# Kernel optimization log

Measured on AMD Instinct MI355X. Metric: run time of the kernel, lower is better.

## Reference

```python
import jax, jax.numpy as jnp
import numpy as np
from jax import lax

B, T, D, NH = 8, 2048, 128, 4
HD = D // NH
EPS = 1e-5


def _ln(x, g, b):
    m = x.mean(-1, keepdims=True)
    v = ((x - m) ** 2).mean(-1, keepdims=True)
    return (x - m) / jnp.sqrt(v + EPS) * g + b


def _gelu(x):  # exact (erf) GELU, matching torch nn.GELU default
    return jax.nn.gelu(x, approximate=False)


def _forward(lob_feat, trade_feat, has_trade,
             ei_w, ei_b, ei_g, ei_beta, decay,
             in_proj_w, in_proj_b, out_proj_w, out_proj_b,
             cn_g, cn_b,
             lob_w, lob_b, lob_g, lob_beta,
             tr_w, tr_b, tr_g, tr_beta,
             of_w, of_b, of_g, of_beta):
    # event impact: Linear -> LayerNorm -> Tanh, gated by has_trade
    impact = jnp.tanh(_ln(trade_feat @ ei_w.T + ei_b, ei_g, ei_beta))
    impact = impact * has_trade[..., None]              # [B,T,D]

    # diagonal linear recurrence: state_t = sigmoid(decay) * state_{t-1} + impact_t
    d = jax.nn.sigmoid(decay)                           # [D]

    def step(s, x):
        s = d * s + x
        return s, s

    _, states = lax.scan(step, jnp.zeros_like(impact[:, 0]),
                         jnp.swapaxes(impact, 0, 1))    # [T,B,D]
    state_seq = jnp.swapaxes(states, 0, 1)              # [B,T,D]

    # fusion MLPs (dropout is identity in eval)
    lob_enh = _gelu(_ln(jnp.concatenate([lob_feat, state_seq], -1) @ lob_w.T + lob_b,
                        lob_g, lob_beta))
    trade_enh = _gelu(_ln(jnp.concatenate([trade_feat, state_seq], -1) @ tr_w.T + tr_b,
                          tr_g, tr_beta))

    # torch nn.MultiheadAttention (batch_first): q=lob_enh, k=v=trade_enh
    wq, wk, wv = in_proj_w[:D], in_proj_w[D:2 * D], in_proj_w[2 * D:]
    bq, bk, bv = in_proj_b[:D], in_proj_b[D:2 * D], in_proj_b[2 * D:]
    q = (lob_enh @ wq.T + bq).reshape(B, T, NH, HD)
    k = (trade_enh @ wk.T + bk).reshape(B, T, NH, HD)
    v = (trade_enh @ wv.T + bv).reshape(B, T, NH, HD)
    scores = jnp.einsum('bqhd,bkhd->bhqk', q, k) / jnp.sqrt(jnp.float32(HD))
    attn = jax.nn.softmax(scores, axis=-1)
    ctx = jnp.einsum('bhqk,bkhd->bqhd', attn, v).reshape(B, T, D)
    fused_attn = ctx @ out_proj_w.T + out_proj_b

    fused = _ln(lob_enh + fused_attn, cn_g, cn_b)
    output = _gelu(_ln(jnp.concatenate([fused, trade_enh], -1) @ of_w.T + of_b,
                       of_g, of_beta))
    return output


def setup_inputs() -> dict:
    key = jax.random.key(0)
    ks = jax.random.split(key, 20)
    s1 = 1.0 / np.sqrt(D)
    s2 = 1.0 / np.sqrt(2 * D)
    return {
        'lob_feat': jax.random.normal(ks[0], (B, T, D), jnp.float32),
        'trade_feat': jax.random.normal(ks[1], (B, T, D), jnp.float32),
        'has_trade': (jax.random.uniform(ks[2], (B, T)) < 0.5).astype(jnp.float32),
        'ei_w': jax.random.normal(ks[3], (D, D), jnp.float32) * s1,
        'ei_b': jnp.zeros((D,), jnp.float32),
        'ei_g': jnp.ones((D,), jnp.float32),
        'ei_beta': jnp.zeros((D,), jnp.float32),
        'decay': jnp.ones((D,), jnp.float32) * 0.9,
        'in_proj_w': jax.random.normal(ks[4], (3 * D, D), jnp.float32) * s1,
        'in_proj_b': jnp.zeros((3 * D,), jnp.float32),
        'out_proj_w': jax.random.normal(ks[5], (D, D), jnp.float32) * s1,
        'out_proj_b': jnp.zeros((D,), jnp.float32),
        'cn_g': jnp.ones((D,), jnp.float32),
        'cn_b': jnp.zeros((D,), jnp.float32),
        'lob_w': jax.random.normal(ks[6], (D, 2 * D), jnp.float32) * s2,
        'lob_b': jnp.zeros((D,), jnp.float32),
        'lob_g': jnp.ones((D,), jnp.float32),
        'lob_beta': jnp.zeros((D,), jnp.float32),
        'tr_w': jax.random.normal(ks[7], (D, 2 * D), jnp.float32) * s2,
        'tr_b': jnp.zeros((D,), jnp.float32),
        'tr_g': jnp.ones((D,), jnp.float32),
        'tr_beta': jnp.zeros((D,), jnp.float32),
        'of_w': jax.random.normal(ks[8], (D, 2 * D), jnp.float32) * s2,
        'of_b': jnp.zeros((D,), jnp.float32),
        'of_g': jnp.ones((D,), jnp.float32),
        'of_beta': jnp.zeros((D,), jnp.float32),
    }


def reference(lob_feat, trade_feat, has_trade,
              ei_w, ei_b, ei_g, ei_beta, decay,
              in_proj_w, in_proj_b, out_proj_w, out_proj_b,
              cn_g, cn_b,
              lob_w, lob_b, lob_g, lob_beta,
              tr_w, tr_b, tr_g, tr_beta,
              of_w, of_b, of_g, of_beta):
    return _forward(lob_feat, trade_feat, has_trade,
                    ei_w, ei_b, ei_g, ei_beta, decay,
                    in_proj_w, in_proj_b, out_proj_w, out_proj_b,
                    cn_g, cn_b,
                    lob_w, lob_b, lob_g, lob_beta,
                    tr_w, tr_b, tr_g, tr_beta,
                    of_w, of_b, of_g, of_beta)
```

## Files before the change

kernel.cpp:

```cpp
#include <hip/hip_runtime.h>
#include <math.h>


#define T_  2048

typedef short bf16x8 __attribute__((ext_vector_type(8)));
typedef float f32x4  __attribute__((ext_vector_type(4)));
typedef unsigned short ushort_t;

__device__ __forceinline__ float sigm(float x) { return 1.0f / (1.0f + __expf(-x)); }

__device__ __forceinline__ unsigned short f2bf(float x) {
    union { float f; unsigned u; } v; v.f = x;
    unsigned r = v.u + 0x7FFFu + ((v.u >> 16) & 1u);
    return (unsigned short)(r >> 16);
}
__device__ __forceinline__ float bf2f(ushort_t u) {
    union { unsigned u; float f; } v; v.u = ((unsigned)u) << 16; return v.f;
}

__device__ __forceinline__ float gelu_f(float x) {
    const float e = exp2f(fmaf(0.044715f * x, x * x, x) * -2.3022083f);
    return x * __builtin_amdgcn_rcpf(1.0f + e);
}
__device__ __forceinline__ float tanh_f(float y) {
    const float e = exp2f(y * 2.8853900818f);
    return 1.0f - 2.0f * __builtin_amdgcn_rcpf(e + 1.0f);
}
#define MX3(a, b, c) fmaxf(fmaxf((a), (b)), (c))

__global__ __launch_bounds__(256) void prep_kernel(
    const float* __restrict__ lob, const float* __restrict__ trade,
    const float* __restrict__ eiw, const float* __restrict__ ipw,
    const float* __restrict__ opw, const float* __restrict__ lobw,
    const float* __restrict__ trw, const float* __restrict__ ofw,
    ushort_t* __restrict__ pool)
{
    const size_t i8 = ((size_t)blockIdx.x * 256 + threadIdx.x) * 8;
    const float* src; size_t off;
    if      (i8 < 2097152) { src = lob;   off = 0; }
    else if (i8 < 4194304) { src = trade; off = 2097152; }
    else if (i8 < 4210688) { src = eiw;   off = 4194304; }
    else if (i8 < 4259840) { src = ipw;   off = 4210688; }
    else if (i8 < 4276224) { src = opw;   off = 4259840; }
    else if (i8 < 4308992) { src = lobw;  off = 4276224; }
    else if (i8 < 4341760) { src = trw;   off = 4308992; }
    else                   { src = ofw;   off = 4341760; }
    const float4 a = *(const float4*)(src + (i8 - off));
    const float4 b = *(const float4*)(src + (i8 - off) + 4);
    bf16x8 o;
    o[0] = (short)f2bf(a.x); o[1] = (short)f2bf(a.y);
    o[2] = (short)f2bf(a.z); o[3] = (short)f2bf(a.w);
    o[4] = (short)f2bf(b.x); o[5] = (short)f2bf(b.y);
    o[6] = (short)f2bf(b.z); o[7] = (short)f2bf(b.w);
    *(bf16x8*)(pool + i8) = o;
}

__global__ __launch_bounds__(256) void gemm_ei(
    const ushort_t* __restrict__ Xb0, const ushort_t* __restrict__ Wb,
    const float* __restrict__ bias, const float* __restrict__ gamma,
    const float* __restrict__ beta, const float* __restrict__ extra,
    ushort_t* __restrict__ outb)
{
    __shared__ float red[32][2][2];
    const int tid = threadIdx.x, wid = tid >> 6, lane = tid & 63;
    const int c2 = lane & 15, g = lane >> 4;
    const int rowblk = wid >> 1, chf = wid & 1, cb0 = chf * 4;
    const int R0 = blockIdx.x * 32 + rowblk * 16;

    f32x4 acc[4] = {};
#pragma unroll
    for (int ch = 0; ch < 4; ch++) {
        const bf16x8 a = *(const bf16x8*)(Xb0 + (size_t)(R0 + c2) * 128 + ch * 32 + g * 8);
#pragma unroll
        for (int j = 0; j < 4; j++) {
            const bf16x8 b = *(const bf16x8*)(Wb + (size_t)((cb0 + j) * 16 + c2) * 128 + ch * 32 + g * 8);
            acc[j] = __builtin_amdgcn_mfma_f32_16x16x32_bf16(a, b, acc[j], 0, 0, 0);
        }
    }
    float gm[4], bt[4];
#pragma unroll
    for (int j = 0; j < 4; j++) {
        const int col = (cb0 + j) * 16 + c2;
        const float bb = bias[col];
        gm[j] = gamma[col]; bt[j] = beta[col];
#pragma unroll
        for (int r = 0; r < 4; r++) acc[j][r] += bb;
    }
#pragma unroll
    for (int r = 0; r < 4; r++) {
        float s = 0.f, ss = 0.f;
#pragma unroll
        for (int j = 0; j < 4; j++) { const float v = acc[j][r]; s += v; ss = fmaf(v, v, ss); }
#pragma unroll
        for (int o = 8; o; o >>= 1) { s += __shfl_xor(s, o); ss += __shfl_xor(ss, o); }
        if (c2 == 0) {
            red[rowblk * 16 + 4 * g + r][chf][0] = s;
            red[rowblk * 16 + 4 * g + r][chf][1] = ss;
        }
    }
    __syncthreads();
#pragma unroll
    for (int r = 0; r < 4; r++) {
        const int lr = rowblk * 16 + 4 * g + r;
        const float S  = red[lr][0][0] + red[lr][1][0];
        const float SS = red[lr][0][1] + red[lr][1][1];
        const float mean = S * (1.0f / 128.0f);
        float var = SS * (1.0f / 128.0f) - mean * mean;
        var = fmaxf(var, 0.0f);
        const float rstd = rsqrtf(var + 1e-5f);
        const int R = blockIdx.x * 32 + lr;
        const float ext = extra[R];
#pragma unroll
        for (int j = 0; j < 4; j++) {
            const float y = (acc[j][r] - mean) * rstd * gm[j] + bt[j];
            outb[(size_t)R * 128 + (cb0 + j) * 16 + c2] = f2bf(tanh_f(y) * ext);
        }
    }
}

__global__ __launch_bounds__(256) void enh_qkv(
    const ushort_t* __restrict__ lobb, const ushort_t* __restrict__ trab,
    const ushort_t* __restrict__ stab,
    const ushort_t* __restrict__ lobw, const ushort_t* __restrict__ trw,
    const ushort_t* __restrict__ ipw, const float* __restrict__ ipb,
    const float* __restrict__ lob_b, const float* __restrict__ lob_g,
    const float* __restrict__ lob_beta,
    const float* __restrict__ tr_b, const float* __restrict__ tr_g,
    const float* __restrict__ tr_beta,
    ushort_t* __restrict__ lobe_b, ushort_t* __restrict__ tre_bf,
    ushort_t* __restrict__ qo, ushort_t* __restrict__ ko, ushort_t* __restrict__ vo)
{
    __shared__ ushort_t lob_t[32][136];
    __shared__ ushort_t tre_t[32][136];
    __shared__ ushort_t vls[128][36];
    __shared__ float red[32][2][4];
    const int tid = threadIdx.x, wid = tid >> 6, lane = tid & 63;
    const int c2 = lane & 15, g = lane >> 4;
    const int rowblk = wid >> 1, chf = wid & 1, cb0 = chf * 4;
    const int RB = blockIdx.x * 32;
    const int R0 = RB + rowblk * 16;

    f32x4 aL[4] = {}, aT[4] = {};
#pragma unroll
    for (int ch = 0; ch < 8; ch++) {
        const int kk = (ch & 3) * 32;
        bf16x8 xl, xt;
        if (ch < 4) {
            xl = *(const bf16x8*)(lobb + (size_t)(R0 + c2) * 128 + kk + g * 8);
            xt = *(const bf16x8*)(trab + (size_t)(R0 + c2) * 128 + kk + g * 8);
        } else {
            xl = *(const bf16x8*)(stab + (size_t)(R0 + c2) * 128 + kk + g * 8);
            xt = xl;
        }
#pragma unroll
        for (int j = 0; j < 4; j++) {
            const size_t wo = (size_t)((cb0 + j) * 16 + c2) * 256 + ch * 32 + g * 8;
            aL[j] = __builtin_amdgcn_mfma_f32_16x16x32_bf16(xl, *(const bf16x8*)(lobw + wo), aL[j], 0, 0, 0);
            aT[j] = __builtin_amdgcn_mfma_f32_16x16x32_bf16(xt, *(const bf16x8*)(trw + wo), aT[j], 0, 0, 0);
        }
    }
#pragma unroll
    for (int j = 0; j < 4; j++) {
        const int col = (cb0 + j) * 16 + c2;
        const float bL = lob_b[col], bT = tr_b[col];
#pragma unroll
        for (int r = 0; r < 4; r++) { aL[j][r] += bL; aT[j][r] += bT; }
    }
#pragma unroll
    for (int r = 0; r < 4; r++) {
        float sL = 0.f, ssL = 0.f, sT = 0.f, ssT = 0.f;
#pragma unroll
        for (int j = 0; j < 4; j++) {
            const float vL = aL[j][r], vT = aT[j][r];
            sL += vL; ssL = fmaf(vL, vL, ssL);
            sT += vT; ssT = fmaf(vT, vT, ssT);
        }
#pragma unroll
        for (int o = 8; o; o >>= 1) {
            sL += __shfl_xor(sL, o); ssL += __shfl_xor(ssL, o);
            sT += __shfl_xor(sT, o); ssT += __shfl_xor(ssT, o);
        }
        if (c2 == 0) {
            float* rd = red[rowblk * 16 + 4 * g + r][chf];
            rd[0] = sL; rd[1] = ssL; rd[2] = sT; rd[3] = ssT;
        }
    }
    __syncthreads();
#pragma unroll
    for (int r = 0; r < 4; r++) {
        const int lr = rowblk * 16 + 4 * g + r;
        const int R = RB + lr;
        const float SL  = red[lr][0][0] + red[lr][1][0];
        const float SSL = red[lr][0][1] + red[lr][1][1];
        const float ST  = red[lr][0][2] + red[lr][1][2];
        const float SST = red[lr][0][3] + red[lr][1][3];
        const float mL = SL * (1.0f / 128.0f), mT = ST * (1.0f / 128.0f);
        const float rL = rsqrtf(fmaxf(SSL * (1.0f / 128.0f) - mL * mL, 0.0f) + 1e-5f);
        const float rT = rsqrtf(fmaxf(SST * (1.0f / 128.0f) - mT * mT, 0.0f) + 1e-5f);
#pragma unroll
        for (int j = 0; j < 4; j++) {
            const int col = (cb0 + j) * 16 + c2;
            const float yL = gelu_f((aL[j][r] - mL) * rL * lob_g[col] + lob_beta[col]);
// ... 3 lines not shown
            lob_t[lr][col] = lb;
            const ushort_t tb = f2bf(yT);
            tre_bf[(size_t)R * 128 + col] = tb;
            tre_t[lr][col] = tb;
        }
    }
    __syncthreads();

    const float qscale = 0.17677669529663687f * 1.4426950408889634f;
#pragma unroll
    for (int which = 0; which < 3; which++) {
        const ushort_t (*src)[136] = (which == 0) ? lob_t : tre_t;
        const ushort_t* Wp = ipw + (size_t)which * 16384;
        f32x4 pa[4] = {};
#pragma unroll
        for (int ch = 0; ch < 4; ch++) {
            const bf16x8 a = *(const bf16x8*)&src[rowblk * 16 + c2][ch * 32 + g * 8];
#pragma unroll
            for (int j = 0; j < 4; j++) {
                const bf16x8 b = *(const bf16x8*)(Wp + (size_t)((cb0 + j) * 16 + c2) * 128 + ch * 32 + g * 8);
                pa[j] = __builtin_amdgcn_mfma_f32_16x16x32_bf16(a, b, pa[j], 0, 0, 0);
            }
        }
        if (which < 2) {
            ushort_t* dst = (which == 0) ? qo : ko;
            const float sc = (which == 0) ? qscale : 1.0f;
#pragma unroll
            for (int j = 0; j < 4; j++) {
                const int col = (cb0 + j) * 16 + c2;
                const float bb = ipb[which * 128 + col];
                const int h = col >> 5, hd = col & 31;
#pragma unroll
                for (int r = 0; r < 4; r++) {
                    const int R = R0 + 4 * g + r;
                    const int b = R >> 11, t = R & 2047;
                    dst[(((size_t)b * 4 + h) * 2048 + t) * 32 + hd] = f2bf((pa[j][r] + bb) * sc);
                }
            }
        } else {
#pragma unroll
            for (int j = 0; j < 4; j++) {
                const int col = (cb0 + j) * 16 + c2;
                const float bb = ipb[256 + col];
#pragma unroll
                for (int r = 0; r < 4; r++)
                    vls[col][rowblk * 16 + 4 * g + r] = f2bf(pa[j][r] + bb);
            }
        }
    }
    __syncthreads();
    {
        const int col = tid >> 1, hf = tid & 1;
        const int h = col >> 5, hd = col & 31;
        const int b = RB >> 11;
        unsigned w[8];
#pragma unroll
        for (int e = 0; e < 8; e++) {
            const int p0 = hf * 16 + 2 * e;
            const int g2 = p0 >> 3, j2 = p0 & 7;
            const int lk = 4 * g2 + j2 + (j2 >= 4 ? 12 : 0);
            w[e] = (unsigned)vls[col][lk] | ((unsigned)vls[col][lk + 1] << 16);
        }
        ushort_t* dst = vo + (((size_t)b * 4 + h) * 32 + hd) * 2048 + (RB & 2047) + hf * 16;
        *(uint4*)dst       = *(const uint4*)&w[0];
        *(uint4*)(dst + 8) = *(const uint4*)&w[4];
    }
}

__global__ __launch_bounds__(256) void attn_kernel(
    const ushort_t* __restrict__ q, const ushort_t* __restrict__ k,
    const ushort_t* __restrict__ vtg,
    ushort_t* __restrict__ part, float* __restrict__ rs_part,
    float* __restrict__ m_part)
{
    __shared__ ushort_t ks[2][64][40];
    __shared__ ushort_t vt[2][32][72];
    const int tid = threadIdx.x, wid = tid >> 6, lane = tid & 63;
    const int c = lane & 15, g = lane >> 4;
    const int half = blockIdx.x & 1, qt = blockIdx.x >> 1;
    const int bh = blockIdx.y, b = bh >> 2, h = bh & 3;
    const ushort_t* kb_ = k   + (size_t)bh * 65536 + (size_t)half * 1024 * 32;
    const ushort_t* vb_ = vtg + (size_t)bh * 65536 + (size_t)half * 1024;
    const int q0 = qt * 128 + wid * 32;

    const ushort_t* qbase = q + ((size_t)bh * 2048 + q0) * 32;
    const bf16x8 qf0 = *(const bf16x8*)(qbase + (size_t)c * 32 + g * 8);
    const bf16x8 qf1 = *(const bf16x8*)(qbase + (size_t)(16 + c) * 32 + g * 8);

    bf16x8 ones;
#pragma unroll
    for (int i = 0; i < 8; i++) ones[i] = (short)0x3F80;

    float m0 = 0.0f, m1 = 0.0f;
    f32x4 acc[2][2] = {};
    f32x4 racc[2] = {};

    const int srow = tid >> 2, ssg = tid & 3;
    const int vd = tid >> 3, vkg = tid & 7;

    {
        const bf16x8 kk8 = *(const bf16x8*)(kb_ + (size_t)srow * 32 + ssg * 8);
        const bf16x8 vv8 = *(const bf16x8*)(vb_ + (size_t)vd * 2048 + vkg * 8);
        *(bf16x8*)&ks[0][srow][ssg * 8] = kk8;
        *(bf16x8*)&vt[0][vd][vkg * 8] = vv8;
    }
    __syncthreads();

    for (int kt = 0; kt < 16; kt++) {
        const int cur = kt & 1;
        bf16x8 kk8, vv8;
        if (kt + 1 < 16) {
            kk8 = *(const bf16x8*)(kb_ + ((size_t)(kt + 1) * 64 + srow) * 32 + ssg * 8);
            vv8 = *(const bf16x8*)(vb_ + (size_t)vd * 2048 + (kt + 1) * 64 + vkg * 8);
        }

        f32x4 s0[4], s1[4];
        __builtin_amdgcn_s_setprio(1);
#pragma unroll
        for (int kb2 = 0; kb2 < 4; kb2++) {
            const bf16x8 kf = *(const bf16x8*)&ks[cur][kb2 * 16 + c][g * 8];
            f32x4 z = {};
            s0[kb2] = __builtin_amdgcn_mfma_f32_16x16x32_bf16(kf, qf0, z, 0, 0, 0);
            s1[kb2] = __builtin_amdgcn_mfma_f32_16x16x32_bf16(kf, qf1, z, 0, 0, 0);
        }
        __builtin_amdgcn_s_setprio(0);

        float lm = MX3(s0[0][0], s0[0][1], s0[0][2]);
        lm = MX3(lm, s0[0][3], s0[1][0]);
        lm = MX3(lm, s0[1][1], s0[1][2]);
        lm = MX3(lm, s0[1][3], s0[2][0]);
        lm = MX3(lm, s0[2][1], s0[2][2]);
        lm = MX3(lm, s0[2][3], s0[3][0]);
        lm = MX3(lm, s0[3][1], s0[3][2]);
        lm = MX3(lm, s0[3][3], s1[0][0]);
        lm = MX3(lm, s1[0][1], s1[0][2]);
        lm = MX3(lm, s1[0][3], s1[1][0]);
        lm = MX3(lm, s1[1][1], s1[1][2]);
        lm = MX3(lm, s1[1][3], s1[2][0]);
        lm = MX3(lm, s1[2][1], s1[2][2]);
        lm = MX3(lm, s1[2][3], s1[3][0]);
        lm = MX3(lm, s1[3][1], s1[3][2]);
        lm = fmaxf(lm, s1[3][3]);
        if (__any(lm > 80.0f || m0 != 0.0f || m1 != 0.0f)) {
            float l0 = -1e30f, l1 = -1e30f;
#pragma unroll
            for (int kb2 = 0; kb2 < 4; kb2++) {
#pragma unroll
                for (int r = 0; r < 4; r++) { l0 = fmaxf(l0, s0[kb2][r]); l1 = fmaxf(l1, s1[kb2][r]); }
            }
            l0 = fmaxf(l0, __shfl_xor(l0, 16)); l0 = fmaxf(l0, __shfl_xor(l0, 32));
            l1 = fmaxf(l1, __shfl_xor(l1, 16)); l1 = fmaxf(l1, __shfl_xor(l1, 32));
            const float n0 = fmaxf(m0, l0), n1 = fmaxf(m1, l1);
            const float a0 = exp2f(m0 - n0), a1 = exp2f(m1 - n1);
#pragma unroll
            for (int nb = 0; nb < 2; nb++)
#pragma unroll
                for (int r = 0; r < 4; r++) { acc[0][nb][r] *= a0; acc[1][nb][r] *= a1; }
#pragma unroll
            for (int r = 0; r < 4; r++) { racc[0][r] *= a0; racc[1][r] *= a1; }
            m0 = n0; m1 = n1;
#pragma unroll
            for (int kb2 = 0; kb2 < 4; kb2++)
#pragma unroll
                for (int r = 0; r < 4; r++) {
                    s0[kb2][r] = exp2f(s0[kb2][r] - m0);
                    s1[kb2][r] = exp2f(s1[kb2][r] - m1);
                }
        } else {
#pragma unroll
            for (int kb2 = 0; kb2 < 4; kb2++)
#pragma unroll
                for (int r = 0; r < 4; r++) {
                    s0[kb2][r] = exp2f(s0[kb2][r]);
                    s1[kb2][r] = exp2f(s1[kb2][r]);
                }
        }

        union { unsigned u[4]; bf16x8 v; } p0a, p0b, p1a, p1b;
        asm("v_cvt_pk_bf16_f32 %0, %1, %2" : "=v"(p0a.u[0]) : "v"(s0[0][0]), "v"(s0[0][1]));
        asm("v_cvt_pk_bf16_f32 %0, %1, %2" : "=v"(p0a.u[1]) : "v"(s0[0][2]), "v"(s0[0][3]));
        asm("v_cvt_pk_bf16_f32 %0, %1, %2" : "=v"(p0a.u[2]) : "v"(s0[1][0]), "v"(s0[1][1]));
        asm("v_cvt_pk_bf16_f32 %0, %1, %2" : "=v"(p0a.u[3]) : "v"(s0[1][2]), "v"(s0[1][3]));
        asm("v_cvt_pk_bf16_f32 %0, %1, %2" : "=v"(p0b.u[0]) : "v"(s0[2][0]), "v"(s0[2][1]));
        asm("v_cvt_pk_bf16_f32 %0, %1, %2" : "=v"(p0b.u[1]) : "v"(s0[2][2]), "v"(s0[2][3]));
        asm("v_cvt_pk_bf16_f32 %0, %1, %2" : "=v"(p0b.u[2]) : "v"(s0[3][0]), "v"(s0[3][1]));
        asm("v_cvt_pk_bf16_f32 %0, %1, %2" : "=v"(p0b.u[3]) : "v"(s0[3][2]), "v"(s0[3][3]));
        asm("v_cvt_pk_bf16_f32 %0, %1, %2" : "=v"(p1a.u[0]) : "v"(s1[0][0]), "v"(s1[0][1]));
        asm("v_cvt_pk_bf16_f32 %0, %1, %2" : "=v"(p1a.u[1]) : "v"(s1[0][2]), "v"(s1[0][3]));
        asm("v_cvt_pk_bf16_f32 %0, %1, %2" : "=v"(p1a.u[2]) : "v"(s1[1][0]), "v"(s1[1][1]));
        asm("v_cvt_pk_bf16_f32 %0, %1, %2" : "=v"(p1a.u[3]) : "v"(s1[1][2]), "v"(s1[1][3]));
        asm("v_cvt_pk_bf16_f32 %0, %1, %2" : "=v"(p1b.u[0]) : "v"(s1[2][0]), "v"(s1[2][1]));
        asm("v_cvt_pk_bf16_f32 %0, %1, %2" : "=v"(p1b.u[1]) : "v"(s1[2][2]), "v"(s1[2][3]));
        asm("v_cvt_pk_bf16_f32 %0, %1, %2" : "=v"(p1b.u[2]) : "v"(s1[3][0]), "v"(s1[3][1]));
        asm("v_cvt_pk_bf16_f32 %0, %1, %2" : "=v"(p1b.u[3]) : "v"(s1[3][2]), "v"(s1[3][3]));

        __builtin_amdgcn_s_setprio(1);
#pragma unroll
        for (int nb = 0; nb < 2; nb++) {
            const bf16x8 v0 = *(const bf16x8*)&vt[cur][nb * 16 + c][g * 8];
            const bf16x8 v1 = *(const bf16x8*)&vt[cur][nb * 16 + c][32 + g * 8];
            acc[0][nb] = __builtin_amdgcn_mfma_f32_16x16x32_bf16(v0, p0a.v, acc[0][nb], 0, 0, 0);
            acc[0][nb] = __builtin_amdgcn_mfma_f32_16x16x32_bf16(v1, p0b.v, acc[0][nb], 0, 0, 0);
            acc[1][nb] = __builtin_amdgcn_mfma_f32_16x16x32_bf16(v0, p1a.v, acc[1][nb], 0, 0, 0);
            acc[1][nb] = __builtin_amdgcn_mfma_f32_16x16x32_bf16(v1, p1b.v, acc[1][nb], 0, 0, 0);
        }
        racc[0] = __builtin_amdgcn_mfma_f32_16x16x32_bf16(ones, p0a.v, racc[0], 0, 0, 0);
        racc[0] = __builtin_amdgcn_mfma_f32_16x16x32_bf16(ones, p0b.v, racc[0], 0, 0, 0);
        racc[1] = __builtin_amdgcn_mfma_f32_16x16x32_bf16(ones, p1a.v, racc[1], 0, 0, 0);
        racc[1] = __builtin_amdgcn_mfma_f32_16x16x32_bf16(ones, p1b.v, racc[1], 0, 0, 0);
        __builtin_amdgcn_s_setprio(0);

        if (kt + 1 < 16) {
            *(bf16x8*)&ks[cur ^ 1][srow][ssg * 8] = kk8;
            *(bf16x8*)&vt[cur ^ 1][vd][vkg * 8] = vv8;
        }
        __syncthreads();
    }

    ushort_t* pb = part + (size_t)half * 2097152;
#pragma unroll
    for (int qf = 0; qf < 2; qf++) {
        const int qrow = q0 + qf * 16 + c;
        ushort_t* dst = pb + ((size_t)(b * 2048 + qrow)) * 128 + h * 32;
#pragma unroll
        for (int nb = 0; nb < 2; nb++) {
            unsigned w0, w1;
            asm("v_cvt_pk_bf16_f32 %0, %1, %2" : "=v"(w0) : "v"(acc[qf][nb][0]), "v"(acc[qf][nb][1]));
            asm("v_cvt_pk_bf16_f32 %0, %1, %2" : "=v"(w1) : "v"(acc[qf][nb][2]), "v"(acc[qf][nb][3]));
            uint2 wv; wv.x = w0; wv.y = w1;
            *(uint2*)(dst + nb * 16 + 4 * g) = wv;
        }
    }
    if (g == 0) {
        float* rsp = rs_part + (size_t)(half * 32 + bh) * 2048;
        float* mp  = m_part  + (size_t)(half * 32 + bh) * 2048;
        rsp[q0 + c]      = racc[0][0];
        rsp[q0 + 16 + c] = racc[1][0];
        mp[q0 + c]       = m0;
        mp[q0 + 16 + c]  = m1;
    }
}

__global__ __launch_bounds__(256) void out_fuse(
    const ushort_t* __restrict__ ctxA, const ushort_t* __restrict__ ctxB,
    const float* __restrict__ rs_part, const float* __restrict__ m_part,
    const ushort_t* __restrict__ treb,
    const ushort_t* __restrict__ opw, const float* __restrict__ opb,
    const float* __restrict__ cn_g, const float* __restrict__ cn_b,
    const ushort_t* __restrict__ ofw, const float* __restrict__ of_b,
    const float* __restrict__ of_g, const float* __restrict__ of_beta,
    const ushort_t* __restrict__ lobe_b, float* __restrict__ out)
{
    __shared__ ushort_t fus_t[32][136];
    __shared__ float red[32][2][2];
    const int tid = threadIdx.x, wid = tid >> 6, lane = tid & 63;
    const int c2 = lane & 15, g = lane >> 4;
    const int rowblk = wid >> 1, chf = wid & 1, cb0 = chf * 4;
    const int RB = blockIdx.x * 32;
    const int R0 = RB + rowblk * 16;

    const int rowA = R0 + c2;
    const int bb2 = rowA >> 11, tt = rowA & 2047;
    float fA[4], fB[4];
#pragma unroll
    for (int h = 0; h < 4; h++) {
        const int bh = bb2 * 4 + h;
        const float mA = m_part[(size_t)bh * 2048 + tt];
        const float mB = m_part[(size_t)(32 + bh) * 2048 + tt];
        const float rA = rs_part[(size_t)bh * 2048 + tt];
        const float rB = rs_part[(size_t)(32 + bh) * 2048 + tt];
        const float M = fmaxf(mA, mB);
        const float wA = exp2f(mA - M), wB = exp2f(mB - M);
        const float inv = __builtin_amdgcn_rcpf(fmaf(rA, wA, rB * wB));
        fA[h] = wA * inv; fB[h] = wB * inv;
    }

    f32x4 acc[4] = {};
#pragma unroll
    for (int ch = 0; ch < 4; ch++) {
        const bf16x8 aA = *(const bf16x8*)(ctxA + (size_t)rowA * 128 + ch * 32 + g * 8);
        const bf16x8 aB = *(const bf16x8*)(ctxB + (size_t)rowA * 128 + ch * 32 + g * 8);
        union { unsigned u[4]; bf16x8 v; } am;
#pragma unroll
        for (int i = 0; i < 4; i++) {
            const float e0 = bf2f((ushort_t)aA[2 * i]) * fA[ch] + bf2f((ushort_t)aB[2 * i]) * fB[ch];
            const float e1 = bf2f((ushort_t)aA[2 * i + 1]) * fA[ch] + bf2f((ushort_t)aB[2 * i + 1]) * fB[ch];
            asm("v_cvt_pk_bf16_f32 %0, %1, %2" : "=v"(am.u[i]) : "v"(e0), "v"(e1));
        }
#pragma unroll
        for (int j = 0; j < 4; j++) {
            const bf16x8 b = *(const bf16x8*)(opw + (size_t)((cb0 + j) * 16 + c2) * 128 + ch * 32 + g * 8);
            acc[j] = __builtin_amdgcn_mfma_f32_16x16x32_bf16(am.v, b, acc[j], 0, 0, 0);
        }
    }
#pragma unroll
    for (int j = 0; j < 4; j++) {
        const int col = (cb0 + j) * 16 + c2;
        const float bb = opb[col];
#pragma unroll
        for (int r = 0; r < 4; r++)
            acc[j][r] += bb + bf2f(lobe_b[(size_t)(R0 + 4 * g + r) * 128 + col]);
    }
#pragma unroll
    for (int r = 0; r < 4; r++) {
        float s = 0.f, ss = 0.f;
#pragma unroll
        for (int j = 0; j < 4; j++) { const float v = acc[j][r]; s += v; ss = fmaf(v, v, ss); }
#pragma unroll
        for (int o = 8; o; o >>= 1) { s += __shfl_xor(s, o); ss += __shfl_xor(ss, o); }
        if (c2 == 0) {
            red[rowblk * 16 + 4 * g + r][chf][0] = s;
            red[rowblk * 16 + 4 * g + r][chf][1] = ss;
        }
    }
    __syncthreads();
#pragma unroll
    for (int r = 0; r < 4; r++) {
        const int lr = rowblk * 16 + 4 * g + r;
        const float S  = red[lr][0][0] + red[lr][1][0];
        const float SS = red[lr][0][1] + red[lr][1][1];
        const float mean = S * (1.0f / 128.0f);
        const float rstd = rsqrtf(fmaxf(SS * (1.0f / 128.0f) - mean * mean, 0.0f) + 1e-5f);
#pragma unroll
        for (int j = 0; j < 4; j++) {
            const int col = (cb0 + j) * 16 + c2;
            fus_t[lr][col] = f2bf((acc[j][r] - mean) * rstd * cn_g[col] + cn_b[col]);
        }
    }
    __syncthreads();

    f32x4 a2[4] = {};
#pragma unroll
    for (int ch = 0; ch < 8; ch++) {
        bf16x8 a;
        if (ch < 4) a = *(const bf16x8*)&fus_t[rowblk * 16 + c2][ch * 32 + g * 8];
        else        a = *(const bf16x8*)(treb + (size_t)(R0 + c2) * 128 + (ch - 4) * 32 + g * 8);
#pragma unroll
        for (int j = 0; j < 4; j++) {
            const bf16x8 b = *(const bf16x8*)(ofw + (size_t)((cb0 + j) * 16 + c2) * 256 + ch * 32 + g * 8);
            a2[j] = __builtin_amdgcn_mfma_f32_16x16x32_bf16(a, b, a2[j], 0, 0, 0);
        }
    }
#pragma unroll
    for (int j = 0; j < 4; j++) {
        const float bb = of_b[(cb0 + j) * 16 + c2];
#pragma unroll
        for (int r = 0; r < 4; r++) a2[j][r] += bb;
    }
#pragma unroll
    for (int r = 0; r < 4; r++) {
        float s = 0.f, ss = 0.f;
#pragma unroll
        for (int j = 0; j < 4; j++) { const float v = a2[j][r]; s += v; ss = fmaf(v, v, ss); }
#pragma unroll
        for (int o = 8; o; o >>= 1) { s += __shfl_xor(s, o); ss += __shfl_xor(ss, o); }
        if (c2 == 0) {
            red[rowblk * 16 + 4 * g + r][chf][0] = s;
            red[rowblk * 16 + 4 * g + r][chf][1] = ss;
        }
    }
    __syncthreads();
#pragma unroll
    for (int r = 0; r < 4; r++) {
        const int lr = rowblk * 16 + 4 * g + r;
        const float S  = red[lr][0][0] + red[lr][1][0];
        const float SS = red[lr][0][1] + red[lr][1][1];
        const float mean = S * (1.0f / 128.0f);
        const float rstd = rsqrtf(fmaxf(SS * (1.0f / 128.0f) - mean * mean, 0.0f) + 1e-5f);
        const int R = RB + lr;
#pragma unroll
        for (int j = 0; j < 4; j++) {
            const int col = (cb0 + j) * 16 + c2;
            const float y = (a2[j][r] - mean) * rstd * of_g[col] + of_beta[col];
            out[(size_t)R * 128 + col] = gelu_f(y);
        }
    }
}

__global__ void scan_ends_kernel(const ushort_t* __restrict__ imp,
                                 const float* __restrict__ decay,
                                 float* __restrict__ ends)
{
    const int c = threadIdx.x;
    const int ch = blockIdx.x, b = blockIdx.y;
    const float d = sigm(decay[c]);
    const size_t base = ((size_t)b * T_ + ch * 64) * 128 + c;
    float s = 0.0f;
#pragma unroll 4
    for (int tl = 0; tl < 64; tl++)
        s = fmaf(d, s, bf2f(imp[base + (size_t)tl * 128]));
    ends[((size_t)b * 32 + ch) * 128 + c] = s;
}

__global__ void scan_carry_kernel(const float* __restrict__ ends,
                                  const float* __restrict__ decay,
                                  float* __restrict__ carry)
{
    const int c = threadIdx.x;
    const int b = blockIdx.x;
    const float d = sigm(decay[c]);
    float dl = d;
#pragma unroll
    for (int i = 0; i < 6; i++) dl *= dl;
    float e = 0.0f;
#pragma unroll
    for (int ch = 0; ch < 32; ch++) {
        carry[((size_t)b * 32 + ch) * 128 + c] = e;
        e = fmaf(dl, e, ends[((size_t)b * 32 + ch) * 128 + c]);
    }
}

__global__ void scan_fin_kernel(const ushort_t* __restrict__ imp,
                                const float* __restrict__ decay,
                                const float* __restrict__ carry,
                                ushort_t* __restrict__ stbf)
{
    const int c = threadIdx.x;
    const int ch = blockIdx.x, b = blockIdx.y;
    const float d = sigm(decay[c]);
    float s = carry[((size_t)b * 32 + ch) * 128 + c];
    const size_t base = ((size_t)b * T_ + ch * 64) * 128 + c;
#pragma unroll 4
    for (int tl = 0; tl < 64; tl++) {
        s = fmaf(d, s, bf2f(imp[base + (size_t)tl * 128]));
        stbf[base + (size_t)tl * 128] = f2bf(s);
    }
}

extern "C" void kernel_launch(void* const* d_in, const int* in_sizes, int n_in,
                              void* d_out, int out_size, void* d_ws, size_t ws_size,
                              hipStream_t stream)
{
    const float* lob_feat   = (const float*)d_in[0];
    const float* trade_feat = (const float*)d_in[1];
    const float* has_trade  = (const float*)d_in[2];
    const float* ei_w       = (const float*)d_in[3];
    const float* ei_b       = (const float*)d_in[4];
    const float* ei_g       = (const float*)d_in[5];
    const float* ei_beta    = (const float*)d_in[6];
    const float* decay      = (const float*)d_in[7];
    const float* in_proj_w  = (const float*)d_in[8];
    const float* in_proj_b  = (const float*)d_in[9];
    const float* out_proj_w = (const float*)d_in[10];
    const float* out_proj_b = (const float*)d_in[11];
    const float* cn_g       = (const float*)d_in[12];
    const float* cn_b       = (const float*)d_in[13];
    const float* lob_w      = (const float*)d_in[14];
    const float* lob_b      = (const float*)d_in[15];
    const float* lob_g      = (const float*)d_in[16];
    const float* lob_beta   = (const float*)d_in[17];
    const float* tr_w       = (const float*)d_in[18];
    const float* tr_b       = (const float*)d_in[19];
    const float* tr_g       = (const float*)d_in[20];
    const float* tr_beta    = (const float*)d_in[21];
    const float* of_w       = (const float*)d_in[22];
    const float* of_b       = (const float*)d_in[23];
    const float* of_g       = (const float*)d_in[24];
    const float* of_beta    = (const float*)d_in[25];

    char* W = (char*)d_ws;
    const size_t MB = 1u << 20;
    ushort_t* lobe_b   = (ushort_t*)W;
    float*    carry    = (float*)(W + 8 * MB);
    float*    ends     = (float*)(W + 8 * MB + 256 * 1024);
    ushort_t* pool     = (ushort_t*)(W + 9 * MB);
    ushort_t* imp_bf   = (ushort_t*)(W + 18 * MB);
    ushort_t* state_bf = (ushort_t*)(W + 22 * MB);
    ushort_t* tre_bf   = (ushort_t*)(W + 26 * MB);
    ushort_t* q_bf     = (ushort_t*)(W + 30 * MB);
    ushort_t* k_bf     = (ushort_t*)(W + 34 * MB);
    ushort_t* vt_g     = (ushort_t*)(W + 38 * MB);
    ushort_t* part     = (ushort_t*)(W + 42 * MB);
    float*    rs_part  = (float*)(W + 50 * MB);
    float*    m_part   = (float*)(W + 50 * MB + 512 * 1024);

    ushort_t* lob_bf   = pool;
    ushort_t* trade_bf = pool + 2097152;
    ushort_t* eiw_bf   = pool + 4194304;
    ushort_t* ipw_bf   = pool + 4210688;
    ushort_t* opw_bf   = pool + 4259840;
    ushort_t* lobw_bf  = pool + 4276224;
    ushort_t* trw_bf   = pool + 4308992;
    ushort_t* ofw_bf   = pool + 4341760;

    ushort_t* ctxA = part;
    ushort_t* ctxB = part + 2097152;

    const dim3 blk(256);

    prep_kernel<<<dim3(2136), blk, 0, stream>>>(lob_feat, trade_feat, ei_w, in_proj_w,
                                                out_proj_w, lob_w, tr_w, of_w, pool);
    gemm_ei<<<dim3(512), blk, 0, stream>>>(trade_bf, eiw_bf, ei_b, ei_g, ei_beta,
                                           has_trade, imp_bf);
    scan_ends_kernel<<<dim3(32, 8), dim3(128), 0, stream>>>(imp_bf, decay, ends);
    scan_carry_kernel<<<dim3(8), dim3(128), 0, stream>>>(ends, decay, carry);
    scan_fin_kernel<<<dim3(32, 8), dim3(128), 0, stream>>>(imp_bf, decay, carry, state_bf);
    enh_qkv<<<dim3(512), blk, 0, stream>>>(lob_bf, trade_bf, state_bf, lobw_bf, trw_bf,
                                           ipw_bf, in_proj_b, lob_b, lob_g, lob_beta,
                                           tr_b, tr_g, tr_beta, lobe_b, tre_bf,
                                           q_bf, k_bf, vt_g);
    attn_kernel<<<dim3(32, 32), blk, 0, stream>>>(q_bf, k_bf, vt_g, part, rs_part, m_part);
    out_fuse<<<dim3(512), blk, 0, stream>>>(ctxA, ctxB, rs_part, m_part, tre_bf,
                                            opw_bf, out_proj_b, cn_g, cn_b,
                                            ofw_bf, of_b, of_g, of_beta, lobe_b, (float*)d_out);
}
```

Before: 139.7 us.

## Fuse input bf16 conversion into GEMMs, merge scan-ends into EI kernel, pre-swizzle V

```diff
diff --git a/kernel.cpp b/kernel.cpp
--- a/kernel.cpp
+++ b/kernel.cpp
@@ -18,6 +18,11 @@
 __device__ __forceinline__ float bf2f(ushort_t u) {
     union { unsigned u; float f; } v; v.u = ((unsigned)u) << 16; return v.f;
 }
+__device__ __forceinline__ unsigned cvtpk(float a, float b) {
+    unsigned r;
+    asm("v_cvt_pk_bf16_f32 %0, %1, %2" : "=v"(r) : "v"(a), "v"(b));
+    return r;
+}
 
 __device__ __forceinline__ float gelu_f(float x) {
     const float e = exp2f(fmaf(0.044715f * x, x * x, x) * -2.3022083f);
@@ -29,8 +34,16 @@
 }
 #define MX3(a, b, c) fmaxf(fmaxf((a), (b)), (c))
 
-__global__ __launch_bounds__(256) void prep_kernel(
-    const float* __restrict__ lob, const float* __restrict__ trade,
+__device__ __forceinline__ bf16x8 ld_f32_bf8(const float* p) {
+    const float4 a = *(const float4*)p;
+    const float4 b = *(const float4*)(p + 4);
+    union { unsigned u[4]; bf16x8 v; } o;
+    o.u[0] = cvtpk(a.x, a.y); o.u[1] = cvtpk(a.z, a.w);
+    o.u[2] = cvtpk(b.x, b.y); o.u[3] = cvtpk(b.z, b.w);
+    return o.v;
+}
+
+__global__ __launch_bounds__(256) void prep_w(
     const float* __restrict__ eiw, const float* __restrict__ ipw,
     const float* __restrict__ opw, const float* __restrict__ lobw,
     const float* __restrict__ trw, const float* __restrict__ ofw,
@@ -38,40 +51,34 @@
 {
     const size_t i8 = ((size_t)blockIdx.x * 256 + threadIdx.x) * 8;
     const float* src; size_t off;
-    if      (i8 < 2097152) { src = lob;   off = 0; }
-    else if (i8 < 4194304) { src = trade; off = 2097152; }
-    else if (i8 < 4210688) { src = eiw;   off = 4194304; }
-    else if (i8 < 4259840) { src = ipw;   off = 4210688; }
-    else if (i8 < 4276224) { src = opw;   off = 4259840; }
-    else if (i8 < 4308992) { src = lobw;  off = 4276224; }
-    else if (i8 < 4341760) { src = trw;   off = 4308992; }
-    else                   { src = ofw;   off = 4341760; }
-    const float4 a = *(const float4*)(src + (i8 - off));
-    const float4 b = *(const float4*)(src + (i8 - off) + 4);
-    bf16x8 o;
-    o[0] = (short)f2bf(a.x); o[1] = (short)f2bf(a.y);
-    o[2] = (short)f2bf(a.z); o[3] = (short)f2bf(a.w);
-    o[4] = (short)f2bf(b.x); o[5] = (short)f2bf(b.y);
-    o[6] = (short)f2bf(b.z); o[7] = (short)f2bf(b.w);
-    *(bf16x8*)(pool + i8) = o;
-}
-
-__global__ __launch_bounds__(256) void gemm_ei(
-    const ushort_t* __restrict__ Xb0, const ushort_t* __restrict__ Wb,
+    if      (i8 < 16384)  { src = eiw;  off = 0; }
+    else if (i8 < 65536)  { src = ipw;  off = 16384; }
+    else if (i8 < 81920)  { src = opw;  off = 65536; }
+    else if (i8 < 114688) { src = lobw; off = 81920; }
+    else if (i8 < 147456) { src = trw;  off = 114688; }
+    else                  { src = ofw;  off = 147456; }
+    *(bf16x8*)(pool + i8) = ld_f32_bf8(src + (i8 - off));
+}
+
+__global__ __launch_bounds__(512) void ei_scan(
+    const float* __restrict__ trade, const ushort_t* __restrict__ Wb,
     const float* __restrict__ bias, const float* __restrict__ gamma,
     const float* __restrict__ beta, const float* __restrict__ extra,
-    ushort_t* __restrict__ outb)
-{
-    __shared__ float red[32][2][2];
+    const float* __restrict__ decay,
+    ushort_t* __restrict__ imp_out, float* __restrict__ ends)
+{
+    __shared__ ushort_t imp_t[64][132];
+    __shared__ float red[64][2][2];
     const int tid = threadIdx.x, wid = tid >> 6, lane = tid & 63;
     const int c2 = lane & 15, g = lane >> 4;
     const int rowblk = wid >> 1, chf = wid & 1, cb0 = chf * 4;
-    const int R0 = blockIdx.x * 32 + rowblk * 16;
+    const int RB = blockIdx.x * 64;
+    const int R0 = RB + rowblk * 16;
 
     f32x4 acc[4] = {};
 #pragma unroll
     for (int ch = 0; ch < 4; ch++) {
-        const bf16x8 a = *(const bf16x8*)(Xb0 + (size_t)(R0 + c2) * 128 + ch * 32 + g * 8);
+        const bf16x8 a = ld_f32_bf8(trade + (size_t)(R0 + c2) * 128 + ch * 32 + g * 8);
 #pragma unroll
         for (int j = 0; j < 4; j++) {
             const bf16x8 b = *(const bf16x8*)(Wb + (size_t)((cb0 + j) * 16 + c2) * 128 + ch * 32 + g * 8);
@@ -106,21 +113,32 @@
         const float S  = red[lr][0][0] + red[lr][1][0];
         const float SS = red[lr][0][1] + red[lr][1][1];
         const float mean = S * (1.0f / 128.0f);
-        float var = SS * (1.0f / 128.0f) - mean * mean;
-        var = fmaxf(var, 0.0f);
-        const float rstd = rsqrtf(var + 1e-5f);
-        const int R = blockIdx.x * 32 + lr;
+        const float rstd = rsqrtf(fmaxf(SS * (1.0f / 128.0f) - mean * mean, 0.0f) + 1e-5f);
+        const int R = RB + lr;
         const float ext = extra[R];
 #pragma unroll
         for (int j = 0; j < 4; j++) {
+            const int col = (cb0 + j) * 16 + c2;
             const float y = (acc[j][r] - mean) * rstd * gm[j] + bt[j];
-            outb[(size_t)R * 128 + (cb0 + j) * 16 + c2] = f2bf(tanh_f(y) * ext);
-        }
+            const ushort_t ib = f2bf(tanh_f(y) * ext);
+            imp_out[(size_t)R * 128 + col] = ib;
+            imp_t[lr][col] = ib;
+        }
+    }
+    __syncthreads();
+    if (tid < 128) {
+        const int c = tid;
+        const float d = sigm(decay[c]);
+        float s = 0.0f;
+#pragma unroll 4
+        for (int tl = 0; tl < 64; tl++) s = fmaf(d, s, bf2f(imp_t[tl][c]));
+        const int b = RB >> 11, ch64 = (RB & 2047) >> 6;
+        ends[((size_t)b * 32 + ch64) * 128 + c] = s;
     }
 }
 
 __global__ __launch_bounds__(256) void enh_qkv(
-    const ushort_t* __restrict__ lobb, const ushort_t* __restrict__ trab,
+    const float* __restrict__ lobf, const float* __restrict__ traf,
     const ushort_t* __restrict__ stab,
     const ushort_t* __restrict__ lobw, const ushort_t* __restrict__ trw,
     const ushort_t* __restrict__ ipw, const float* __restrict__ ipb,
@@ -129,7 +147,7 @@
     const float* __restrict__ tr_b, const float* __restrict__ tr_g,
     const float* __restrict__ tr_beta,
     ushort_t* __restrict__ lobe_b, ushort_t* __restrict__ tre_bf,
-    ushort_t* __restrict__ qo, ushort_t* __restrict__ ko, ushort_t* __restrict__ vo)
+    ushort_t* __restrict__ qo, ushort_t* __restrict__ ko, ushort_t* __restrict__ vo2)
 {
     __shared__ ushort_t lob_t[32][136];
     __shared__ ushort_t tre_t[32][136];
@@ -147,8 +165,8 @@
         const int kk = (ch & 3) * 32;
         bf16x8 xl, xt;
         if (ch < 4) {
-            xl = *(const bf16x8*)(lobb + (size_t)(R0 + c2) * 128 + kk + g * 8);
-            xt = *(const bf16x8*)(trab + (size_t)(R0 + c2) * 128 + kk + g * 8);
+            xl = ld_f32_bf8(lobf + (size_t)(R0 + c2) * 128 + kk + g * 8);
+            xt = ld_f32_bf8(traf + (size_t)(R0 + c2) * 128 + kk + g * 8);
         } else {
             xl = *(const bf16x8*)(stab + (size_t)(R0 + c2) * 128 + kk + g * 8);
             xt = xl;
@@ -258,35 +276,39 @@
     {
         const int col = tid >> 1, hf = tid & 1;
         const int h = col >> 5, hd = col & 31;
+        const int nb = hd >> 4, c = hd & 15;
         const int b = RB >> 11;
-        unsigned w[8];
-#pragma unroll
-        for (int e = 0; e < 8; e++) {
-            const int p0 = hf * 16 + 2 * e;
-            const int g2 = p0 >> 3, j2 = p0 & 7;
-            const int lk = 4 * g2 + j2 + (j2 >= 4 ? 12 : 0);
-            w[e] = (unsigned)vls[col][lk] | ((unsigned)vls[col][lk + 1] << 16);
-        }
-        ushort_t* dst = vo + (((size_t)b * 4 + h) * 32 + hd) * 2048 + (RB & 2047) + hf * 16;
-        *(uint4*)dst       = *(const uint4*)&w[0];
-        *(uint4*)(dst + 8) = *(const uint4*)&w[4];
+        const int t0 = RB & 2047;
+        const int kt = t0 >> 6, kh = (t0 >> 5) & 1;
+        ushort_t* fbase = vo2 + ((size_t)(b * 4 + h)) * 65536 + kt * 2048 + kh * 1024 + nb * 512;
+#pragma unroll
+        for (int gp2 = 0; gp2 < 2; gp2++) {
+            const int gp = 2 * hf + gp2;
+            unsigned w[4];
+#pragma unroll
+            for (int e = 0; e < 4; e++) {
+                const int p = gp * 8 + 2 * e;
+                const int j2 = p & 7;
+                const int lk = 4 * (p >> 3) + j2 + (j2 >= 4 ? 12 : 0);
+                w[e] = (unsigned)vls[col][lk] | ((unsigned)vls[col][lk + 1] << 16);
+            }
+            *(uint4*)(fbase + gp * 128 + c * 8) = *(const uint4*)&w[0];
+        }
     }
 }
 
 __global__ __launch_bounds__(256) void attn_kernel(
     const ushort_t* __restrict__ q, const ushort_t* __restrict__ k,
-    const ushort_t* __restrict__ vtg,
+    const ushort_t* __restrict__ v2,
     ushort_t* __restrict__ part, float* __restrict__ rs_part,
     float* __restrict__ m_part)
 {
-    __shared__ ushort_t ks[2][64][40];
-    __shared__ ushort_t vt[2][32][72];
     const int tid = threadIdx.x, wid = tid >> 6, lane = tid & 63;
     const int c = lane & 15, g = lane >> 4;
     const int half = blockIdx.x & 1, qt = blockIdx.x >> 1;
     const int bh = blockIdx.y, b = bh >> 2, h = bh & 3;
-    const ushort_t* kb_ = k   + (size_t)bh * 65536 + (size_t)half * 1024 * 32;
-    const ushort_t* vb_ = vtg + (size_t)bh * 65536 + (size_t)half * 1024;
+    const ushort_t* kb_ = k  + (size_t)bh * 65536 + (size_t)half * 32768;
+    const ushort_t* vt_ = v2 + (size_t)bh * 65536 + (size_t)half * 32768;
     const int q0 = qt * 128 + wid * 32;
 
     const ushort_t* qbase = q + ((size_t)bh * 2048 + q0) * 32;
@@ -301,59 +323,36 @@
     f32x4 acc[2][2] = {};
     f32x4 racc[2] = {};
 
-    const int srow = tid >> 2, ssg = tid & 3;
-    const int vd = tid >> 3, vkg = tid & 7;
-
-    {
-        const bf16x8 kk8 = *(const bf16x8*)(kb_ + (size_t)srow * 32 + ssg * 8);
-        const bf16x8 vv8 = *(const bf16x8*)(vb_ + (size_t)vd * 2048 + vkg * 8);
-        *(bf16x8*)&ks[0][srow][ssg * 8] = kk8;
-        *(bf16x8*)&vt[0][vd][vkg * 8] = vv8;
-    }
-    __syncthreads();
-
     for (int kt = 0; kt < 16; kt++) {
-        const int cur = kt & 1;
-        bf16x8 kk8, vv8;
-        if (kt + 1 < 16) {
-            kk8 = *(const bf16x8*)(kb_ + ((size_t)(kt + 1) * 64 + srow) * 32 + ssg * 8);
-            vv8 = *(const bf16x8*)(vb_ + (size_t)vd * 2048 + (kt + 1) * 64 + vkg * 8);
-        }
-
         f32x4 s0[4], s1[4];
         __builtin_amdgcn_s_setprio(1);
 #pragma unroll
         for (int kb2 = 0; kb2 < 4; kb2++) {
-            const bf16x8 kf = *(const bf16x8*)&ks[cur][kb2 * 16 + c][g * 8];
+            const bf16x8 kf = *(const bf16x8*)(kb_ + ((size_t)(kt * 64 + kb2 * 16 + c)) * 32 + g * 8);
             f32x4 z = {};
             s0[kb2] = __builtin_amdgcn_mfma_f32_16x16x32_bf16(kf, qf0, z, 0, 0, 0);
             s1[kb2] = __builtin_amdgcn_mfma_f32_16x16x32_bf16(kf, qf1, z, 0, 0, 0);
         }
         __builtin_amdgcn_s_setprio(0);
 
-        float lm = MX3(s0[0][0], s0[0][1], s0[0][2]);
-        lm = MX3(lm, s0[0][3], s0[1][0]);
-        lm = MX3(lm, s0[1][1], s0[1][2]);
-        lm = MX3(lm, s0[1][3], s0[2][0]);
-        lm = MX3(lm, s0[2][1], s0[2][2]);
-        lm = MX3(lm, s0[2][3], s0[3][0]);
-        lm = MX3(lm, s0[3][1], s0[3][2]);
-        lm = MX3(lm, s0[3][3], s1[0][0]);
-        lm = MX3(lm, s1[0][1], s1[0][2]);
-        lm = MX3(lm, s1[0][3], s1[1][0]);
-        lm = MX3(lm, s1[1][1], s1[1][2]);
-        lm = MX3(lm, s1[1][3], s1[2][0]);
-        lm = MX3(lm, s1[2][1], s1[2][2]);
-        lm = MX3(lm, s1[2][3], s1[3][0]);
-        lm = MX3(lm, s1[3][1], s1[3][2]);
-        lm = fmaxf(lm, s1[3][3]);
+        const float t0 = MX3(s0[0][0], s0[0][1], s0[0][2]);
+        const float t1 = MX3(s0[0][3], s0[1][0], s0[1][1]);
+        const float t2 = MX3(s0[1][2], s0[1][3], s0[2][0]);
+        const float t3 = MX3(s0[2][1], s0[2][2], s0[2][3]);
+        const float t4 = MX3(s0[3][0], s0[3][1], s0[3][2]);
+        const float u0 = MX3(s1[0][0], s1[0][1], s1[0][2]);
+        const float u1 = MX3(s1[0][3], s1[1][0], s1[1][1]);
+        const float u2 = MX3(s1[1][2], s1[1][3], s1[2][0]);
+        const float u3 = MX3(s1[2][1], s1[2][2], s1[2][3]);
+        const float u4 = MX3(s1[3][0], s1[3][1], s1[3][2]);
+        const float lm = fmaxf(MX3(MX3(t0, t1, t2), MX3(t3, t4, s0[3][3]), u0),
+                               MX3(MX3(u1, u2, u3), u4, s1[3][3]));
         if (__any(lm > 80.0f || m0 != 0.0f || m1 != 0.0f)) {
             float l0 = -1e30f, l1 = -1e30f;
 #pragma unroll
-            for (int kb2 = 0; kb2 < 4; kb2++) {
+            for (int kb2 = 0; kb2 < 4; kb2++)
 #pragma unroll
                 for (int r = 0; r < 4; r++) { l0 = fmaxf(l0, s0[kb2][r]); l1 = fmaxf(l1, s1[kb2][r]); }
-            }
             l0 = fmaxf(l0, __shfl_xor(l0, 16)); l0 = fmaxf(l0, __shfl_xor(l0, 32));
             l1 = fmaxf(l1, __shfl_xor(l1, 16)); l1 = fmaxf(l1, __shfl_xor(l1, 32));
             const float n0 = fmaxf(m0, l0), n1 = fmaxf(m1, l1);
@@ -383,44 +382,31 @@
         }
 
         union { unsigned u[4]; bf16x8 v; } p0a, p0b, p1a, p1b;
-        asm("v_cvt_pk_bf16_f32 %0, %1, %2" : "=v"(p0a.u[0]) : "v"(s0[0][0]), "v"(s0[0][1]));
-        asm("v_cvt_pk_bf16_f32 %0, %1, %2" : "=v"(p0a.u[1]) : "v"(s0[0][2]), "v"(s0[0][3]));
-        asm("v_cvt_pk_bf16_f32 %0, %1, %2" : "=v"(p0a.u[2]) : "v"(s0[1][0]), "v"(s0[1][1]));
-        asm("v_cvt_pk_bf16_f32 %0, %1, %2" : "=v"(p0a.u[3]) : "v"(s0[1][2]), "v"(s0[1][3]));
-        asm("v_cvt_pk_bf16_f32 %0, %1, %2" : "=v"(p0b.u[0]) : "v"(s0[2][0]), "v"(s0[2][1]));
-        asm("v_cvt_pk_bf16_f32 %0, %1, %2" : "=v"(p0b.u[1]) : "v"(s0[2][2]), "v"(s0[2][3]));
-        asm("v_cvt_pk_bf16_f32 %0, %1, %2" : "=v"(p0b.u[2]) : "v"(s0[3][0]), "v"(s0[3][1]));
-        asm("v_cvt_pk_bf16_f32 %0, %1, %2" : "=v"(p0b.u[3]) : "v"(s0[3][2]), "v"(s0[3][3]));
-        asm("v_cvt_pk_bf16_f32 %0, %1, %2" : "=v"(p1a.u[0]) : "v"(s1[0][0]), "v"(s1[0][1]));
-        asm("v_cvt_pk_bf16_f32 %0, %1, %2" : "=v"(p1a.u[1]) : "v"(s1[0][2]), "v"(s1[0][3]));
-        asm("v_cvt_pk_bf16_f32 %0, %1, %2" : "=v"(p1a.u[2]) : "v"(s1[1][0]), "v"(s1[1][1]));
-        asm("v_cvt_pk_bf16_f32 %0, %1, %2" : "=v"(p1a.u[3]) : "v"(s1[1][2]), "v"(s1[1][3]));
-        asm("v_cvt_pk_bf16_f32 %0, %1, %2" : "=v"(p1b.u[0]) : "v"(s1[2][0]), "v"(s1[2][1]));
-        asm("v_cvt_pk_bf16_f32 %0, %1, %2" : "=v"(p1b.u[1]) : "v"(s1[2][2]), "v"(s1[2][3]));
-        asm("v_cvt_pk_bf16_f32 %0, %1, %2" : "=v"(p1b.u[2]) : "v"(s1[3][0]), "v"(s1[3][1]));
-        asm("v_cvt_pk_bf16_f32 %0, %1, %2" : "=v"(p1b.u[3]) : "v"(s1[3][2]), "v"(s1[3][3]));
-
+        p0a.u[0] = cvtpk(s0[0][0], s0[0][1]); p0a.u[1] = cvtpk(s0[0][2], s0[0][3]);
+        p0a.u[2] = cvtpk(s0[1][0], s0[1][1]); p0a.u[3] = cvtpk(s0[1][2], s0[1][3]);
+        p0b.u[0] = cvtpk(s0[2][0], s0[2][1]); p0b.u[1] = cvtpk(s0[2][2], s0[2][3]);
+        p0b.u[2] = cvtpk(s0[3][0], s0[3][1]); p0b.u[3] = cvtpk(s0[3][2], s0[3][3]);
+        p1a.u[0] = cvtpk(s1[0][0], s1[0][1]); p1a.u[1] = cvtpk(s1[0][2], s1[0][3]);
+        p1a.u[2] = cvtpk(s1[1][0], s1[1][1]); p1a.u[3] = cvtpk(s1[1][2], s1[1][3]);
+        p1b.u[0] = cvtpk(s1[2][0], s1[2][1]); p1b.u[1] = cvtpk(s1[2][2], s1[2][3]);
+        p1b.u[2] = cvtpk(s1[3][0], s1[3][1]); p1b.u[3] = cvtpk(s1[3][2], s1[3][3]);
+
+        const ushort_t* vtile = vt_ + (size_t)kt * 2048;
         __builtin_amdgcn_s_setprio(1);
 #pragma unroll
         for (int nb = 0; nb < 2; nb++) {
-            const bf16x8 v0 = *(const bf16x8*)&vt[cur][nb * 16 + c][g * 8];
-            const bf16x8 v1 = *(const bf16x8*)&vt[cur][nb * 16 + c][32 + g * 8];
-            acc[0][nb] = __builtin_amdgcn_mfma_f32_16x16x32_bf16(v0, p0a.v, acc[0][nb], 0, 0, 0);
-            acc[0][nb] = __builtin_amdgcn_mfma_f32_16x16x32_bf16(v1, p0b.v, acc[0][nb], 0, 0, 0);
-            acc[1][nb] = __builtin_amdgcn_mfma_f32_16x16x32_bf16(v0, p1a.v, acc[1][nb], 0, 0, 0);
-            acc[1][nb] = __builtin_amdgcn_mfma_f32_16x16x32_bf16(v1, p1b.v, acc[1][nb], 0, 0, 0);
+            const bf16x8 vfA = *(const bf16x8*)(vtile + nb * 512 + lane * 8);
+            const bf16x8 vfB = *(const bf16x8*)(vtile + 1024 + nb * 512 + lane * 8);
+            acc[0][nb] = __builtin_amdgcn_mfma_f32_16x16x32_bf16(vfA, p0a.v, acc[0][nb], 0, 0, 0);
+            acc[0][nb] = __builtin_amdgcn_mfma_f32_16x16x32_bf16(vfB, p0b.v, acc[0][nb], 0, 0, 0);
+            acc[1][nb] = __builtin_amdgcn_mfma_f32_16x16x32_bf16(vfA, p1a.v, acc[1][nb], 0, 0, 0);
+            acc[1][nb] = __builtin_amdgcn_mfma_f32_16x16x32_bf16(vfB, p1b.v, acc[1][nb], 0, 0, 0);
         }
         racc[0] = __builtin_amdgcn_mfma_f32_16x16x32_bf16(ones, p0a.v, racc[0], 0, 0, 0);
         racc[0] = __builtin_amdgcn_mfma_f32_16x16x32_bf16(ones, p0b.v, racc[0], 0, 0, 0);
         racc[1] = __builtin_amdgcn_mfma_f32_16x16x32_bf16(ones, p1a.v, racc[1], 0, 0, 0);
         racc[1] = __builtin_amdgcn_mfma_f32_16x16x32_bf16(ones, p1b.v, racc[1], 0, 0, 0);
         __builtin_amdgcn_s_setprio(0);
-
-        if (kt + 1 < 16) {
-            *(bf16x8*)&ks[cur ^ 1][srow][ssg * 8] = kk8;
-            *(bf16x8*)&vt[cur ^ 1][vd][vkg * 8] = vv8;
-        }
-        __syncthreads();
     }
 
     ushort_t* pb = part + (size_t)half * 2097152;
@@ -430,10 +416,9 @@
         ushort_t* dst = pb + ((size_t)(b * 2048 + qrow)) * 128 + h * 32;
 #pragma unroll
         for (int nb = 0; nb < 2; nb++) {
-            unsigned w0, w1;
-            asm("v_cvt_pk_bf16_f32 %0, %1, %2" : "=v"(w0) : "v"(acc[qf][nb][0]), "v"(acc[qf][nb][1]));
-            asm("v_cvt_pk_bf16_f32 %0, %1, %2" : "=v"(w1) : "v"(acc[qf][nb][2]), "v"(acc[qf][nb][3]));
-            uint2 wv; wv.x = w0; wv.y = w1;
+            uint2 wv;
+            wv.x = cvtpk(acc[qf][nb][0], acc[qf][nb][1]);
+            wv.y = cvtpk(acc[qf][nb][2], acc[qf][nb][3]);
             *(uint2*)(dst + nb * 16 + 4 * g) = wv;
         }
     }
@@ -491,7 +476,7 @@
         for (int i = 0; i < 4; i++) {
             const float e0 = bf2f((ushort_t)aA[2 * i]) * fA[ch] + bf2f((ushort_t)aB[2 * i]) * fB[ch];
             const float e1 = bf2f((ushort_t)aA[2 * i + 1]) * fA[ch] + bf2f((ushort_t)aB[2 * i + 1]) * fB[ch];
-            asm("v_cvt_pk_bf16_f32 %0, %1, %2" : "=v"(am.u[i]) : "v"(e0), "v"(e1));
+            am.u[i] = cvtpk(e0, e1);
         }
 #pragma unroll
         for (int j = 0; j < 4; j++) {
@@ -581,21 +566,6 @@
             out[(size_t)R * 128 + col] = gelu_f(y);
         }
     }
-}
-
-__global__ void scan_ends_kernel(const ushort_t* __restrict__ imp,
-                                 const float* __restrict__ decay,
-                                 float* __restrict__ ends)
-{
-    const int c = threadIdx.x;
-    const int ch = blockIdx.x, b = blockIdx.y;
-    const float d = sigm(decay[c]);
-    const size_t base = ((size_t)b * T_ + ch * 64) * 128 + c;
-    float s = 0.0f;
-#pragma unroll 4
-    for (int tl = 0; tl < 64; tl++)
-        s = fmaf(d, s, bf2f(imp[base + (size_t)tl * 128]));
-    ends[((size_t)b * 32 + ch) * 128 + c] = s;
 }
 
 __global__ void scan_carry_kernel(const float* __restrict__ ends,
@@ -667,45 +637,41 @@
     char* W = (char*)d_ws;
     const size_t MB = 1u << 20;
     ushort_t* lobe_b   = (ushort_t*)W;
-    float*    carry    = (float*)(W + 8 * MB);
-    float*    ends     = (float*)(W + 8 * MB + 256 * 1024);
-    ushort_t* pool     = (ushort_t*)(W + 9 * MB);
-    ushort_t* imp_bf   = (ushort_t*)(W + 18 * MB);
-    ushort_t* state_bf = (ushort_t*)(W + 22 * MB);
-    ushort_t* tre_bf   = (ushort_t*)(W + 26 * MB);
-    ushort_t* q_bf     = (ushort_t*)(W + 30 * MB);
-    ushort_t* k_bf     = (ushort_t*)(W + 34 * MB);
-    ushort_t* vt_g     = (ushort_t*)(W + 38 * MB);
-    ushort_t* part     = (ushort_t*)(W + 42 * MB);
-    float*    rs_part  = (float*)(W + 50 * MB);
-    float*    m_part   = (float*)(W + 50 * MB + 512 * 1024);
-
-    ushort_t* lob_bf   = pool;
-    ushort_t* trade_bf = pool + 2097152;
-    ushort_t* eiw_bf   = pool + 4194304;
-    ushort_t* ipw_bf   = pool + 4210688;
-    ushort_t* opw_bf   = pool + 4259840;
-    ushort_t* lobw_bf  = pool + 4276224;
-    ushort_t* trw_bf   = pool + 4308992;
-    ushort_t* ofw_bf   = pool + 4341760;
+    ushort_t* state_bf = (ushort_t*)(W + 4 * MB);
+    ushort_t* tre_bf   = (ushort_t*)(W + 8 * MB);
+    ushort_t* q_bf     = (ushort_t*)(W + 12 * MB);
+    ushort_t* k_bf     = (ushort_t*)(W + 16 * MB);
+    ushort_t* v2       = (ushort_t*)(W + 20 * MB);
+    ushort_t* pool     = (ushort_t*)(W + 24 * MB);
+    float*    carry    = (float*)(W + 25 * MB);
+    float*    ends     = (float*)(W + 25 * MB + 256 * 1024);
+    ushort_t* imp_bf   = (ushort_t*)(W + 26 * MB);
+    ushort_t* part     = (ushort_t*)(W + 30 * MB);
+    float*    rs_part  = (float*)(W + 38 * MB);
+    float*    m_part   = (float*)(W + 38 * MB + 512 * 1024);
+
+    ushort_t* eiw_bf   = pool;
+    ushort_t* ipw_bf   = pool + 16384;
+    ushort_t* opw_bf   = pool + 65536;
+    ushort_t* lobw_bf  = pool + 81920;
+    ushort_t* trw_bf   = pool + 114688;
+    ushort_t* ofw_bf   = pool + 147456;
 
     ushort_t* ctxA = part;
     ushort_t* ctxB = part + 2097152;
 
     const dim3 blk(256);
 
-    prep_kernel<<<dim3(2136), blk, 0, stream>>>(lob_feat, trade_feat, ei_w, in_proj_w,
-                                                out_proj_w, lob_w, tr_w, of_w, pool);
-    gemm_ei<<<dim3(512), blk, 0, stream>>>(trade_bf, eiw_bf, ei_b, ei_g, ei_beta,
-                                           has_trade, imp_bf);
-    scan_ends_kernel<<<dim3(32, 8), dim3(128), 0, stream>>>(imp_bf, decay, ends);
+    prep_w<<<dim3(88), blk, 0, stream>>>(ei_w, in_proj_w, out_proj_w, lob_w, tr_w, of_w, pool);
+    ei_scan<<<dim3(256), dim3(512), 0, stream>>>(trade_feat, eiw_bf, ei_b, ei_g, ei_beta,
+                                                 has_trade, decay, imp_bf, ends);
     scan_carry_kernel<<<dim3(8), dim3(128), 0, stream>>>(ends, decay, carry);
     scan_fin_kernel<<<dim3(32, 8), dim3(128), 0, stream>>>(imp_bf, decay, carry, state_bf);
-    enh_qkv<<<dim3(512), blk, 0, stream>>>(lob_bf, trade_bf, state_bf, lobw_bf, trw_bf,
+    enh_qkv<<<dim3(512), blk, 0, stream>>>(lob_feat, trade_feat, state_bf, lobw_bf, trw_bf,
                                            ipw_bf, in_proj_b, lob_b, lob_g, lob_beta,
                                            tr_b, tr_g, tr_beta, lobe_b, tre_bf,
-                                           q_bf, k_bf, vt_g);
-    attn_kernel<<<dim3(32, 32), blk, 0, stream>>>(q_bf, k_bf, vt_g, part, rs_part, m_part);
+                                           q_bf, k_bf, v2);
+    attn_kernel<<<dim3(32, 32), blk, 0, stream>>>(q_bf, k_bf, v2, part, rs_part, m_part);
     out_fuse<<<dim3(512), blk, 0, stream>>>(ctxA, ctxB, rs_part, m_part, tre_bf,
                                             opw_bf, out_proj_b, cn_g, cn_b,
                                             ofw_bf, of_b, of_g, of_beta, lobe_b, (float*)d_out);
```

Result: slower. 161.0 us (+15.3%).
